# Optimization experiments

Measured on AMD Instinct MI355X. Metric: run time of the kernel, lower is better.

The kernel has to match this reference:

```python
import jax, jax.numpy as jnp
import numpy as np

NUM_HEADS = 12


def setup_inputs() -> dict:
    key = jax.random.key(0)
    ks = jax.random.split(key, 5)
    B, N, C = 2, 256, 768
    x = jax.random.normal(ks[0], (B, N, C), dtype=jnp.float32)
    d = jax.random.normal(ks[1], (B, N, N, C), dtype=jnp.float32)
    w_qkv = jax.random.normal(ks[2], (3 * C, C), dtype=jnp.float32) * 0.02
    w_proj = jax.random.normal(ks[3], (C, C), dtype=jnp.float32) * 0.02
    b_proj = jnp.zeros((C,), dtype=jnp.float32)
    return {"x": x, "d": d, "w_qkv": w_qkv, "w_proj": w_proj, "b_proj": b_proj}


def reference(x, d, w_qkv, w_proj, b_proj):
    B, N, C = x.shape
    H = NUM_HEADS
    hd = C // H
    scale = hd ** -0.5
    # qkv projection (no bias, matching qkv_bias=False)
    qkv = x @ w_qkv.T                                   # [B, N, 3C]
    qkv = qkv.reshape(B, N, 3, H, hd).transpose(2, 0, 3, 1, 4)  # [3, B, H, N, hd]
    q, k, v = qkv[0] * scale, qkv[1], qkv[2]
    attn = jax.nn.softmax(jnp.einsum('bhid,bhjd->bhij', q, k), axis=-1)
    # pairwise bias per head: d -> [B, H, N, N, hd]
    dh = d.reshape(B, N, N, H, hd).transpose(0, 3, 1, 2, 4)
    # sum_j attn[...,j] * (v[j] + d[i,j]) split into the two terms
    out = jnp.einsum('bhij,bhjd->bhid', attn, v) \
        + jnp.einsum('bhij,bhijd->bhid', attn, dh)       # [B, H, N, hd]
    out = out.transpose(0, 2, 1, 3).reshape(B, N, C)
    return out @ w_proj.T + b_proj
```

## Files before the change

kernel.cpp:

```cpp
#include <hip/hip_runtime.h>

typedef __bf16 bf16_t;
typedef bf16_t bf16x8 __attribute__((ext_vector_type(8)));
typedef bf16_t bf16x4 __attribute__((ext_vector_type(4)));
typedef float f32x4 __attribute__((ext_vector_type(4)));

__global__ void f2b_all(const float* __restrict__ x, const float* __restrict__ wq,
                        const float* __restrict__ wp,
                        bf16_t* __restrict__ xb, bf16_t* __restrict__ wqb,
                        bf16_t* __restrict__ wpb) {
    int i = blockIdx.x * blockDim.x + threadIdx.x;
    const float* src; bf16_t* dst; int off;
    if (i < 98304)       { src = x;  dst = xb;  off = i; }
    else if (i < 540672) { src = wq; dst = wqb; off = i - 98304; }
    else                 { src = wp; dst = wpb; off = i - 540672; }
    f32x4 v = reinterpret_cast<const f32x4*>(src)[off];
    bf16x4 o = { (bf16_t)v[0], (bf16_t)v[1], (bf16_t)v[2], (bf16_t)v[3] };
    reinterpret_cast<bf16x4*>(dst)[off] = o;
}

template <typename OUT_T, bool HAS_BIAS>
__global__ __launch_bounds__(256) void gemm_bt(
    const bf16_t* __restrict__ A, const bf16_t* __restrict__ B,
    OUT_T* __restrict__ C, const float* __restrict__ bias,
    int K, int lda, int ldb, int ldc)
{
    const int m0 = blockIdx.x * 64;
    const int n0 = blockIdx.y * 64;

    __shared__ __align__(16) bf16_t As[64][72];
    __shared__ __align__(16) bf16_t Bs[64][72];

    const int tid  = threadIdx.x;
    const int lane = tid & 63;
    const int wave = tid >> 6;

    f32x4 acc[4] = {};

    for (int k0 = 0; k0 < K; k0 += 64) {
#pragma unroll
        for (int c = 0; c < 2; ++c) {
            const int chunk = c * 256 + tid;
            const int row = chunk >> 3;
            const int off = (chunk & 7) * 8;
            *reinterpret_cast<uint4*>(&As[row][off]) =
                *reinterpret_cast<const uint4*>(&A[(long)(m0 + row) * lda + k0 + off]);
            *reinterpret_cast<uint4*>(&Bs[row][off]) =
                *reinterpret_cast<const uint4*>(&B[(long)(n0 + row) * ldb + k0 + off]);
        }
        __syncthreads();
#pragma unroll
        for (int ks = 0; ks < 64; ks += 32) {
            bf16x8 af = *reinterpret_cast<const bf16x8*>(&As[wave * 16 + (lane & 15)][(lane >> 4) * 8 + ks]);
#pragma unroll
            for (int nf = 0; nf < 4; ++nf) {
                bf16x8 bfr = *reinterpret_cast<const bf16x8*>(&Bs[nf * 16 + (lane & 15)][(lane >> 4) * 8 + ks]);
                acc[nf] = __builtin_amdgcn_mfma_f32_16x16x32_bf16(af, bfr, acc[nf], 0, 0, 0);
            }
        }
        __syncthreads();
    }

    const int crow0 = m0 + wave * 16 + (lane >> 4) * 4;
    const int ccol0 = n0 + (lane & 15);
#pragma unroll
    for (int nf = 0; nf < 4; ++nf) {
        const int col = ccol0 + nf * 16;
        const float bv = HAS_BIAS ? bias[col] : 0.0f;
#pragma unroll
        for (int v = 0; v < 4; ++v) {
            C[(long)(crow0 + v) * ldc + col] = (OUT_T)(acc[nf][v] + bv);
        }
    }
}

__global__ __launch_bounds__(256) void qk_softmax(
    const bf16_t* __restrict__ qkv,
    float* __restrict__ probs)
{
    const int bh = blockIdx.y;
    const int b = bh / 12, h = bh % 12;
    const int m0 = blockIdx.x * 64;
    const bf16_t* qbase = qkv + (long)b * 589824 + h * 64;
    const bf16_t* kbase = qkv + (long)b * 589824 + 768 + h * 64;

    __shared__ __align__(16) bf16_t Qs[64][72];
    __shared__ __align__(16) bf16_t Ks[256][72];

    const int t = threadIdx.x;
#pragma unroll
    for (int c = 0; c < 2; ++c) {
        const int chunk = c * 256 + t;
        const int row = chunk >> 3, off = (chunk & 7) * 8;
        *reinterpret_cast<uint4*>(&Qs[row][off]) =
            *reinterpret_cast<const uint4*>(qbase + (long)(m0 + row) * 2304 + off);
    }
#pragma unroll
    for (int c = 0; c < 8; ++c) {
        const int chunk = c * 256 + t;
        const int row = chunk >> 3, off = (chunk & 7) * 8;
        *reinterpret_cast<uint4*>(&Ks[row][off]) =
            *reinterpret_cast<const uint4*>(kbase + (long)row * 2304 + off);
    }
    __syncthreads();

    const int lane = t & 63, wave = t >> 6;
    f32x4 acc[16] = {};
#pragma unroll
    for (int ks = 0; ks < 64; ks += 32) {
        bf16x8 af = *reinterpret_cast<const bf16x8*>(&Qs[wave * 16 + (lane & 15)][(lane >> 4) * 8 + ks]);
#pragma unroll
        for (int nf = 0; nf < 16; ++nf) {
            bf16x8 bfr = *reinterpret_cast<const bf16x8*>(&Ks[nf * 16 + (lane & 15)][(lane >> 4) * 8 + ks]);
            acc[nf] = __builtin_amdgcn_mfma_f32_16x16x32_bf16(af, bfr, acc[nf], 0, 0, 0);
        }
    }

    float inv[4];
#pragma unroll
    for (int v = 0; v < 4; ++v) {
        float mm = -1e30f;
#pragma unroll
        for (int nf = 0; nf < 16; ++nf) { acc[nf][v] *= 0.125f; mm = fmaxf(mm, acc[nf][v]); }
#pragma unroll
        for (int o = 1; o < 16; o <<= 1) mm = fmaxf(mm, __shfl_xor(mm, o));
        float s = 0.0f;
#pragma unroll
        for (int nf = 0; nf < 16; ++nf) { float e = __expf(acc[nf][v] - mm); acc[nf][v] = e; s += e; }
#pragma unroll
        for (int o = 1; o < 16; o <<= 1) s += __shfl_xor(s, o);
        inv[v] = 1.0f / s;
    }

    float* prow = probs + ((long)bh * 256 + m0 + wave * 16 + (lane >> 4) * 4) * 256 + (lane & 15);
#pragma unroll
    for (int nf = 0; nf < 16; ++nf) {
#pragma unroll
        for (int v = 0; v < 4; ++v) {
            prow[(long)v * 256 + nf * 16] = acc[nf][v] * inv[v];
        }
    }
}

__global__ __launch_bounds__(256) void attnd_kernel(
    const float* __restrict__ attn,
    const bf16_t* __restrict__ qkv,
    const float* __restrict__ d,
    bf16_t* __restrict__ oh)
{
    const int bi = blockIdx.x;
    const int b  = bi >> 8;
    const int i  = bi & 255;
    const int cc = blockIdx.y;
    const int t  = threadIdx.x;
    const int lane = t & 63, wave = t >> 6;

    __shared__ float attn_s[4 * 257];
    __shared__ f32x4 partial[3][64];

#pragma unroll
    for (int q = 0; q < 4; ++q) {
        attn_s[q * 257 + t] = attn[(((long)(b * 12 + cc * 4 + q)) * 256 + i) * 256 + t];
    }
    __syncthreads();

    const int c0 = cc * 256 + lane * 4;
    const float* arow = attn_s + (lane >> 4) * 257;
    const int jb = wave * 64;
    const f32x4* dp = reinterpret_cast<const f32x4*>(d + (long)bi * 196608 + (long)jb * 768 + c0);
    const bf16_t* vp = qkv + (long)b * 589824 + (long)jb * 2304 + 1536 + c0;

    f32x4 acc = {};
#pragma unroll 8
    for (int jj = 0; jj < 64; ++jj) {
        f32x4 dv = __builtin_nontemporal_load(dp + (long)jj * 192);
        bf16x4 vv = *reinterpret_cast<const bf16x4*>(vp + (long)jj * 2304);
        float a = arow[jb + jj];
        acc[0] = fmaf(a, dv[0] + (float)vv[0], acc[0]);
        acc[1] = fmaf(a, dv[1] + (float)vv[1], acc[1]);
        acc[2] = fmaf(a, dv[2] + (float)vv[2], acc[2]);
        acc[3] = fmaf(a, dv[3] + (float)vv[3], acc[3]);
    }

    if (wave) partial[wave - 1][lane] = acc;
    __syncthreads();
    if (wave == 0) {
        acc += partial[0][lane] + partial[1][lane] + partial[2][lane];
        bf16x4 o = { (bf16_t)acc[0], (bf16_t)acc[1], (bf16_t)acc[2], (bf16_t)acc[3] };
        *reinterpret_cast<bf16x4*>(oh + (long)bi * 768 + c0) = o;
    }
}

extern "C" void kernel_launch(void* const* d_in, const int* in_sizes, int n_in,
                              void* d_out, int out_size, void* d_ws, size_t ws_size,
                              hipStream_t stream) {
    const float* x      = (const float*)d_in[0];
    const float* d      = (const float*)d_in[1];
    const float* w_qkv  = (const float*)d_in[2];
    const float* w_proj = (const float*)d_in[3];
    const float* b_proj = (const float*)d_in[4];
    float* out = (float*)d_out;

    char* ws = (char*)d_ws;
    bf16_t* xb    = (bf16_t*)(ws);
    bf16_t* wqb   = (bf16_t*)(ws + 786432);
    bf16_t* wpb   = (bf16_t*)(ws + 4325376);
    bf16_t* qkvb  = (bf16_t*)(ws + 5505024);
    float*  probs = (float*)(ws + 7864320);
    bf16_t* oh    = (bf16_t*)(ws + 14155776);

    f2b_all<<<2688, 256, 0, stream>>>(x, w_qkv, w_proj, xb, wqb, wpb);

    gemm_bt<bf16_t, false><<<dim3(8, 36), 256, 0, stream>>>(
        xb, wqb, qkvb, nullptr, 768, 768, 768, 2304);

    qk_softmax<<<dim3(4, 24), 256, 0, stream>>>(qkvb, probs);

    attnd_kernel<<<dim3(512, 3), 256, 0, stream>>>(probs, qkvb, d, oh);

    gemm_bt<float, true><<<dim3(8, 12), 256, 0, stream>>>(
        oh, wpb, out, b_proj, 768, 768, 768, 768);
}
```

Measured before the change: 119.9 us.

## Merge attention-d kernel channel blocks into one 1024-thread block per row

The attn·(v+d) kernel now uses one 1024-thread block per (batch, query) row covering all 768 channels, instead of three 256-thread blocks each covering 256 channels. Each of the 16 waves handles 16 key positions across three channel groups, and partial sums are reduced through a 16×768 shared-memory buffer. The aim is to load the attention rows once per query row and give each thread more independent loads in flight for the bandwidth-bound stream over d. In exchange there are fewer, larger blocks (512 total) with heavy LDS use, which may lower occupancy and lengthen the final reduction.

```diff
diff --git a/kernel.cpp b/kernel.cpp
--- a/kernel.cpp
+++ b/kernel.cpp
@@ -142,7 +142,7 @@
     }
 }
 
-__global__ __launch_bounds__(256) void attnd_kernel(
+__global__ __launch_bounds__(1024) void attnd_kernel(
     const float* __restrict__ attn,
     const bf16_t* __restrict__ qkv,
     const float* __restrict__ d,
@@ -151,43 +151,58 @@
     const int bi = blockIdx.x;
     const int b  = bi >> 8;
     const int i  = bi & 255;
-    const int cc = blockIdx.y;
     const int t  = threadIdx.x;
     const int lane = t & 63, wave = t >> 6;
 
-    __shared__ float attn_s[4 * 257];
-    __shared__ f32x4 partial[3][64];
-
-#pragma unroll
-    for (int q = 0; q < 4; ++q) {
-        attn_s[q * 257 + t] = attn[(((long)(b * 12 + cc * 4 + q)) * 256 + i) * 256 + t];
+    __shared__ float attn_s[12 * 257];
+    __shared__ float pw[16][768];
+
+#pragma unroll
+    for (int it = 0; it < 3; ++it) {
+        const int idx = it * 1024 + t;
+        const int h = idx >> 8, j = idx & 255;
+        attn_s[h * 257 + j] = attn[(((long)(b * 12 + h)) * 256 + i) * 256 + j];
     }
     __syncthreads();
 
-    const int c0 = cc * 256 + lane * 4;
-    const float* arow = attn_s + (lane >> 4) * 257;
-    const int jb = wave * 64;
-    const f32x4* dp = reinterpret_cast<const f32x4*>(d + (long)bi * 196608 + (long)jb * 768 + c0);
-    const bf16_t* vp = qkv + (long)b * 589824 + (long)jb * 2304 + 1536 + c0;
-
-    f32x4 acc = {};
-#pragma unroll 8
-    for (int jj = 0; jj < 64; ++jj) {
-        f32x4 dv = __builtin_nontemporal_load(dp + (long)jj * 192);
-        bf16x4 vv = *reinterpret_cast<const bf16x4*>(vp + (long)jj * 2304);
-        float a = arow[jb + jj];
-        acc[0] = fmaf(a, dv[0] + (float)vv[0], acc[0]);
-        acc[1] = fmaf(a, dv[1] + (float)vv[1], acc[1]);
-        acc[2] = fmaf(a, dv[2] + (float)vv[2], acc[2]);
-        acc[3] = fmaf(a, dv[3] + (float)vv[3], acc[3]);
-    }
-
-    if (wave) partial[wave - 1][lane] = acc;
+    const int h0 = lane >> 4;
+    const float* dbase = d + (long)bi * 196608 + lane * 4;
+    const bf16_t* vbase = qkv + (long)b * 589824 + 1536 + lane * 4;
+    const float* a0p = attn_s + (0 + h0) * 257;
+    const float* a1p = attn_s + (4 + h0) * 257;
+    const float* a2p = attn_s + (8 + h0) * 257;
+
+    f32x4 acc0 = {}, acc1 = {}, acc2 = {};
+#pragma unroll 4
+    for (int jj = 0; jj < 16; ++jj) {
+        const int j = wave * 16 + jj;
+        const float* dr = dbase + (long)j * 768;
+        const bf16_t* vr = vbase + (long)j * 2304;
+        f32x4 d0 = __builtin_nontemporal_load(reinterpret_cast<const f32x4*>(dr));
+        f32x4 d1 = __builtin_nontemporal_load(reinterpret_cast<const f32x4*>(dr + 256));
+        f32x4 d2 = __builtin_nontemporal_load(reinterpret_cast<const f32x4*>(dr + 512));
+        bf16x4 v0 = *reinterpret_cast<const bf16x4*>(vr);
+        bf16x4 v1 = *reinterpret_cast<const bf16x4*>(vr + 256);
+        bf16x4 v2 = *reinterpret_cast<const bf16x4*>(vr + 512);
+        const float a0 = a0p[j], a1 = a1p[j], a2 = a2p[j];
+#pragma unroll
+        for (int e = 0; e < 4; ++e) {
+            acc0[e] = fmaf(a0, d0[e] + (float)v0[e], acc0[e]);
+            acc1[e] = fmaf(a1, d1[e] + (float)v1[e], acc1[e]);
+            acc2[e] = fmaf(a2, d2[e] + (float)v2[e], acc2[e]);
+        }
+    }
+
+    *reinterpret_cast<f32x4*>(&pw[wave][lane * 4])       = acc0;
+    *reinterpret_cast<f32x4*>(&pw[wave][256 + lane * 4]) = acc1;
+    *reinterpret_cast<f32x4*>(&pw[wave][512 + lane * 4]) = acc2;
     __syncthreads();
-    if (wave == 0) {
-        acc += partial[0][lane] + partial[1][lane] + partial[2][lane];
-        bf16x4 o = { (bf16_t)acc[0], (bf16_t)acc[1], (bf16_t)acc[2], (bf16_t)acc[3] };
-        *reinterpret_cast<bf16x4*>(oh + (long)bi * 768 + c0) = o;
+
+    if (t < 768) {
+        float s = 0.0f;
+#pragma unroll
+        for (int w = 0; w < 16; ++w) s += pw[w][t];
+        oh[(long)bi * 768 + t] = (bf16_t)s;
     }
 }
 
@@ -216,7 +231,7 @@
 
     qk_softmax<<<dim3(4, 24), 256, 0, stream>>>(qkvb, probs);
 
-    attnd_kernel<<<dim3(512, 3), 256, 0, stream>>>(probs, qkvb, d, oh);
+    attnd_kernel<<<512, 1024, 0, stream>>>(probs, qkvb, d, oh);
 
     gemm_bt<float, true><<<dim3(8, 12), 256, 0, stream>>>(
         oh, wpb, out, b_proj, 768, 768, 768, 768);
```

Measured after the change: 123.8 us. 1.03x slower.

## Fuse fp32-to-bf16 conversion into GEMM loads and prefetch next K tile

Applied to the files above, without the earlier changes.

Removes the separate conversion kernel by letting the GEMM read fp32 inputs and weights and convert them to bf16 while staging into shared memory. It also adds register double-buffering, so the next K tile's global loads are issued before the current tile's MFMAs. This saves one launch and the write and reread of the bf16 copies. In exchange the GEMMs read twice as many bytes per element, since the weights are now loaded as fp32.

```diff
diff --git a/kernel.cpp b/kernel.cpp
--- a/kernel.cpp
+++ b/kernel.cpp
@@ -5,23 +5,20 @@
 typedef bf16_t bf16x4 __attribute__((ext_vector_type(4)));
 typedef float f32x4 __attribute__((ext_vector_type(4)));
 
-__global__ void f2b_all(const float* __restrict__ x, const float* __restrict__ wq,
-                        const float* __restrict__ wp,
-                        bf16_t* __restrict__ xb, bf16_t* __restrict__ wqb,
-                        bf16_t* __restrict__ wpb) {
-    int i = blockIdx.x * blockDim.x + threadIdx.x;
-    const float* src; bf16_t* dst; int off;
-    if (i < 98304)       { src = x;  dst = xb;  off = i; }
-    else if (i < 540672) { src = wq; dst = wqb; off = i - 98304; }
-    else                 { src = wp; dst = wpb; off = i - 540672; }
-    f32x4 v = reinterpret_cast<const f32x4*>(src)[off];
-    bf16x4 o = { (bf16_t)v[0], (bf16_t)v[1], (bf16_t)v[2], (bf16_t)v[3] };
-    reinterpret_cast<bf16x4*>(dst)[off] = o;
-}
-
-template <typename OUT_T, bool HAS_BIAS>
+__device__ inline bf16x8 ld8(const float* p) {
+    f32x4 a = *reinterpret_cast<const f32x4*>(p);
+    f32x4 b = *reinterpret_cast<const f32x4*>(p + 4);
+    bf16x8 r = { (bf16_t)a[0], (bf16_t)a[1], (bf16_t)a[2], (bf16_t)a[3],
+                 (bf16_t)b[0], (bf16_t)b[1], (bf16_t)b[2], (bf16_t)b[3] };
+    return r;
+}
+__device__ inline bf16x8 ld8(const bf16_t* p) {
+    return *reinterpret_cast<const bf16x8*>(p);
+}
+
+template <typename AT, typename BT, typename OUT_T, bool HAS_BIAS>
 __global__ __launch_bounds__(256) void gemm_bt(
-    const bf16_t* __restrict__ A, const bf16_t* __restrict__ B,
+    const AT* __restrict__ A, const BT* __restrict__ B,
     OUT_T* __restrict__ C, const float* __restrict__ bias,
     int K, int lda, int ldb, int ldc)
 {
@@ -34,21 +31,31 @@
     const int tid  = threadIdx.x;
     const int lane = tid & 63;
     const int wave = tid >> 6;
+    const int srow = tid >> 3;
+    const int soff = (tid & 7) * 8;
+
+    bf16x8 rA0, rA1, rB0, rB1;
+    rA0 = ld8(&A[(long)(m0 + srow)      * lda + soff]);
+    rA1 = ld8(&A[(long)(m0 + srow + 32) * lda + soff]);
+    rB0 = ld8(&B[(long)(n0 + srow)      * ldb + soff]);
+    rB1 = ld8(&B[(long)(n0 + srow + 32) * ldb + soff]);
 
     f32x4 acc[4] = {};
 
     for (int k0 = 0; k0 < K; k0 += 64) {
-#pragma unroll
-        for (int c = 0; c < 2; ++c) {
-            const int chunk = c * 256 + tid;
-            const int row = chunk >> 3;
-            const int off = (chunk & 7) * 8;
-            *reinterpret_cast<uint4*>(&As[row][off]) =
-                *reinterpret_cast<const uint4*>(&A[(long)(m0 + row) * lda + k0 + off]);
-            *reinterpret_cast<uint4*>(&Bs[row][off]) =
-                *reinterpret_cast<const uint4*>(&B[(long)(n0 + row) * ldb + k0 + off]);
-        }
+        *reinterpret_cast<bf16x8*>(&As[srow][soff])      = rA0;
+        *reinterpret_cast<bf16x8*>(&As[srow + 32][soff]) = rA1;
+        *reinterpret_cast<bf16x8*>(&Bs[srow][soff])      = rB0;
+        *reinterpret_cast<bf16x8*>(&Bs[srow + 32][soff]) = rB1;
         __syncthreads();
+
+        if (k0 + 64 < K) {
+            rA0 = ld8(&A[(long)(m0 + srow)      * lda + k0 + 64 + soff]);
+            rA1 = ld8(&A[(long)(m0 + srow + 32) * lda + k0 + 64 + soff]);
+            rB0 = ld8(&B[(long)(n0 + srow)      * ldb + k0 + 64 + soff]);
+            rB1 = ld8(&B[(long)(n0 + srow + 32) * ldb + k0 + 64 + soff]);
+        }
+
 #pragma unroll
         for (int ks = 0; ks < 64; ks += 32) {
             bf16x8 af = *reinterpret_cast<const bf16x8*>(&As[wave * 16 + (lane & 15)][(lane >> 4) * 8 + ks]);
@@ -202,22 +209,17 @@
     float* out = (float*)d_out;
 
     char* ws = (char*)d_ws;
-    bf16_t* xb    = (bf16_t*)(ws);
-    bf16_t* wqb   = (bf16_t*)(ws + 786432);
-    bf16_t* wpb   = (bf16_t*)(ws + 4325376);
     bf16_t* qkvb  = (bf16_t*)(ws + 5505024);
     float*  probs = (float*)(ws + 7864320);
     bf16_t* oh    = (bf16_t*)(ws + 14155776);
 
-    f2b_all<<<2688, 256, 0, stream>>>(x, w_qkv, w_proj, xb, wqb, wpb);
-
-    gemm_bt<bf16_t, false><<<dim3(8, 36), 256, 0, stream>>>(
-        xb, wqb, qkvb, nullptr, 768, 768, 768, 2304);
+    gemm_bt<float, float, bf16_t, false><<<dim3(8, 36), 256, 0, stream>>>(
+        x, w_qkv, qkvb, nullptr, 768, 768, 768, 2304);
 
     qk_softmax<<<dim3(4, 24), 256, 0, stream>>>(qkvb, probs);
 
     attnd_kernel<<<dim3(512, 3), 256, 0, stream>>>(probs, qkvb, d, oh);
 
-    gemm_bt<float, true><<<dim3(8, 12), 256, 0, stream>>>(
-        oh, wpb, out, b_proj, 768, 768, 768, 768);
-}
+    gemm_bt<bf16_t, float, float, true><<<dim3(8, 12), 256, 0, stream>>>(
+        oh, w_proj, out, b_proj, 768, 768, 768, 768);
+}
```

New measurement: 103.0 us. 1.16x faster.
